# Optimization experiments

Measured on AMD Instinct MI355X. Metric: run time of the kernel, lower is better.

The kernel has to match this reference:

```python
import jax, jax.numpy as jnp
import numpy as np

B, SD, AD, M, MAXC = 65536, 32, 1, 32, 2  # batch, state_dim, action_dim, msg_dim, max_children


def _l2norm(x):
    # F.normalize(x, dim=-1) with eps=1e-12
    return x / jnp.maximum(jnp.linalg.norm(x, axis=-1, keepdims=True), 1e-12)


def _mlp(x, w1, b1, w2, b2, w3, b3):
    # MLPBase: Linear->ReLU->Linear->ReLU->Linear (400/300 hidden)
    h = jax.nn.relu(x @ w1 + b1)
    h = jax.nn.relu(h @ w2 + b2)
    return h @ w3 + b3


def setup_inputs() -> dict:
    key = jax.random.key(0)
    ks = iter(jax.random.split(key, 40))

    def p(shape):
        return jax.random.normal(next(ks), shape, jnp.float32) * 0.05

    inp = {
        "state": jax.random.normal(next(ks), (B, SD), jnp.float32),
        "action": jax.random.normal(next(ks), (B, AD), jnp.float32),
        # CriticUp params
        "up_fc1_w": p((SD + AD, 64)), "up_fc1_b": p((64,)),
        "up_fc2_w": p((64 + M, 64)), "up_fc2_b": p((64,)),
        "up_fc3_w": p((64, M)), "up_fc3_b": p((M,)),
        "att_w": p((9 + SD, M)), "att_b": p((M,)),
    }
    q_in = 12 + M + AD + M   # rel_pos(12) + self_input(msg_dim) + action + msg_down
    m_in = 12 + M + M        # rel_pos(12) + self_input + msg_down
    for n, d, out in (("q1", q_in, 1), ("q2", q_in, 1), ("msg", m_in, M * MAXC)):
        inp[n + "_w1"] = p((d, 400)); inp[n + "_b1"] = p((400,))
        inp[n + "_w2"] = p((400, 300)); inp[n + "_b2"] = p((300,))
        inp[n + "_w3"] = p((300, out)); inp[n + "_b3"] = p((out,))
    return inp


def reference(state, action,
              up_fc1_w, up_fc1_b, up_fc2_w, up_fc2_b, up_fc3_w, up_fc3_b,
              att_w, att_b,
              q1_w1, q1_b1, q1_w2, q1_b2, q1_w3, q1_b3,
              q2_w1, q2_b1, q2_w2, q2_b2, q2_w3, q2_b3,
              msg_w1, msg_b1, msg_w2, msg_b2, msg_w3, msg_b3):
    b = state.shape[0]
    # ---- bottom-up (num_limbs=1: root has no children -> zero child states/messages) ----
    xu = _l2norm(jnp.concatenate([state, action], -1) @ up_fc1_w + up_fc1_b)  # [b,64]
    ch_states = jnp.zeros((b, MAXC, 9 + SD), state.dtype)
    att = jax.nn.softmax(ch_states @ att_w + att_b, axis=-2)                  # [b,MAXC,M]
    m_up = (jnp.zeros((b, MAXC, M), state.dtype) * att).sum(-2)              # [b,M] (zeros)
    h = jnp.tanh(jnp.concatenate([xu, m_up], -1))
    h = jnp.tanh(h @ up_fc2_w + up_fc2_b)
    msg_up = _l2norm(h @ up_fc3_w + up_fc3_b)                                 # [b,M]
    # ---- top-down (root's parent index -1 wraps to itself -> zero relative offsets) ----
    pos = state[:, :3]
    rel = jnp.concatenate([jnp.zeros((b, 6), state.dtype), pos, pos], -1)     # [b,12]
    m_td = jnp.zeros((b, M), state.dtype)                                     # sliced from zero parent_msg
    xum = jnp.concatenate([rel, msg_up, action, m_td], -1)
    x1 = _mlp(xum, q1_w1, q1_b1, q1_w2, q1_b2, q1_w3, q1_b3)                  # [b,1]
    x2 = _mlp(xum, q2_w1, q2_b1, q2_w2, q2_b2, q2_w3, q2_b3)                  # [b,1]
    xm = jnp.tanh(jnp.concatenate([rel, msg_up, m_td], -1))
    msg_down = _l2norm(_mlp(xm, msg_w1, msg_b1, msg_w2, msg_b2, msg_w3, msg_b3))
    del msg_down  # computed per torch forward but unused in single-limb output
    # stack over 1 limb then sum over limb dim == identity
    return (x1, x2)
```

## Files before the change

### kernel.cpp

```cpp
#include <hip/hip_runtime.h>
#include <math.h>


#define BTOT   65536
#define XUM_OFF 655360ull

#define PK_BLK  78
#define PH_THR  512
#define PH_ROWS 128
#define PH_BLK  (BTOT / PH_ROWS)
#define F1W 0
#define F1B 2112
#define F2W 2176
#define F2B 6272
#define F3W 6336
#define F3B 8384
#define W0_FLOATS 8416

#define ML_THR  1024
#define ML_ROWS 128
#define ML_BLK  (BTOT / ML_ROWS)
#define H1S     424

typedef float  f32x4 __attribute__((ext_vector_type(4)));
typedef __bf16 bf16x8 __attribute__((ext_vector_type(8)));
typedef unsigned short u16x8 __attribute__((ext_vector_type(8)));
typedef unsigned short u16x4 __attribute__((ext_vector_type(4)));
typedef unsigned int   u32x2 __attribute__((ext_vector_type(2)));

__device__ __forceinline__ unsigned short f2b(float f) {
  union { float f; unsigned int u; } v; v.f = f;
  return (unsigned short)((v.u + 0x7fffu + ((v.u >> 16) & 1u)) >> 16);
}
__device__ __forceinline__ float b2f(unsigned short u) {
  union { unsigned int u; float f; } v; v.u = ((unsigned int)u) << 16;
  return v.f;
}
__device__ __forceinline__ f32x4 MFMA(bf16x8 a, bf16x8 b, f32x4 c) {
  return __builtin_amdgcn_mfma_f32_16x16x32_bf16(a, b, c, 0, 0, 0);
}
__device__ __forceinline__ bf16x8 ld8(const unsigned short* p) {
  return __builtin_bit_cast(bf16x8, *(const u16x8*)p);
}
__device__ __forceinline__ float ftanh(float x) {
  float e = __builtin_amdgcn_exp2f(x * 2.885390081777927f);
  return (e - 1.0f) * __builtin_amdgcn_rcpf(e + 1.0f);
}

struct P0 {
  const float* state; const float* action;
  const float* f1w; const float* f1b;
  const float* f2w; const float* f2b;
  const float* f3w; const float* f3b;
  const float* q1w1; const float* q1b1; const float* q1w2;
  const float* q2w1; const float* q2b1; const float* q2w2;
  unsigned short* ws;
  unsigned short* xum;
};

__global__ __launch_bounds__(PH_THR, 4) void phase0_kernel(P0 P) {
  __shared__ float w0[W0_FLOATS];
  __shared__ unsigned short hx[PH_ROWS * 68];
  const int tid = threadIdx.x;

  if (blockIdx.x < PK_BLK) {
    const int gid = blockIdx.x * PH_THR + tid;
    const int lane = gid & 63, f = gid >> 6;
    const int q = f / 312, fl = f - q * 312;
    const float* w1 = q ? P.q2w1 : P.q1w1;
    const float* b1 = q ? P.q2b1 : P.q1b1;
    const float* w2 = q ? P.q2w2 : P.q1w2;
    int nt, ks; const bool isw1 = (fl < 52);
    if (isw1) { nt = fl >> 1; ks = fl & 1; }
    else      { int fl2 = fl - 52; nt = fl2 / 13; ks = fl2 - nt * 13; }
    const int col = nt * 16 + (lane & 15);
    const int k0  = ks * 32 + (lane >> 4) * 8;
    unsigned short v[8];
    #pragma unroll
    for (int j = 0; j < 8; ++j) {
      const int k = k0 + j;
      float x = 0.f;
      if (isw1) {
        if (col < 400) {
          if (k < 39) x = w1[(6 + k) * 400 + col];
          else if (k == 39) x = b1[col];
        }
      } else {
        if (k < 400 && col < 300) x = w2[k * 300 + col];
      }
      v[j] = f2b(x);
    }
    *(u16x8*)(P.ws + (size_t)f * 512 + lane * 8) = *(const u16x8*)v;
    return;
  }

  const int row = tid >> 2, sub = tid & 3, j0 = sub * 16;
  const long grow = (long)(blockIdx.x - PK_BLK) * PH_ROWS + row;

  for (int i = tid; i < 528;  i += PH_THR) *(f32x4*)(w0 + F1W + 4*i) = *(const f32x4*)(P.f1w + 4*i);
  for (int i = tid; i < 16;   i += PH_THR) *(f32x4*)(w0 + F1B + 4*i) = *(const f32x4*)(P.f1b + 4*i);
  for (int i = tid; i < 1024; i += PH_THR) *(f32x4*)(w0 + F2W + 4*i) = *(const f32x4*)(P.f2w + 4*i);
  for (int i = tid; i < 16;   i += PH_THR) *(f32x4*)(w0 + F2B + 4*i) = *(const f32x4*)(P.f2b + 4*i);
  for (int i = tid; i < 512;  i += PH_THR) *(f32x4*)(w0 + F3W + 4*i) = *(const f32x4*)(P.f3w + 4*i);
  for (int i = tid; i < 8;    i += PH_THR) *(f32x4*)(w0 + F3B + 4*i) = *(const f32x4*)(P.f3b + 4*i);

  float sa[33];
  {
    const float4* sp = (const float4*)(P.state + grow * 32);
    #pragma unroll
    for (int c = 0; c < 8; ++c) {
      float4 v = sp[c];
      sa[c*4+0] = v.x; sa[c*4+1] = v.y; sa[c*4+2] = v.z; sa[c*4+3] = v.w;
    }
    sa[32] = P.action[grow];
  }
  __syncthreads();

  float acc[16];
  #pragma unroll
  for (int j = 0; j < 16; ++j) acc[j] = w0[F1B + j0 + j];
  #pragma unroll 4
  for (int i = 0; i < 33; ++i) {
    const float s = sa[i];
    const f32x4* wr = (const f32x4*)&w0[F1W + i * 64 + j0];
    #pragma unroll
    for (int c = 0; c < 4; ++c) {
      f32x4 wv = wr[c];
      acc[c*4+0] += s * wv[0]; acc[c*4+1] += s * wv[1];
      acc[c*4+2] += s * wv[2]; acc[c*4+3] += s * wv[3];
    }
  }
  {
    float ss = 0.f;
    #pragma unroll
    for (int j = 0; j < 16; ++j) ss += acc[j] * acc[j];
    ss += __shfl_xor(ss, 1, 64); ss += __shfl_xor(ss, 2, 64);
    const float sc = 1.f / fmaxf(sqrtf(ss), 1e-12f);
    #pragma unroll
    for (int j = 0; j < 16; ++j) hx[row * 68 + j0 + j] = f2b(ftanh(acc[j] * sc));
  }
  __syncthreads();
  #pragma unroll
  for (int j = 0; j < 16; ++j) acc[j] = w0[F2B + j0 + j];
  #pragma unroll 4
  for (int i0 = 0; i0 < 16; ++i0) {
    const u16x4 hv4 = *(const u16x4*)&hx[row * 68 + i0 * 4];
    #pragma unroll
    for (int u = 0; u < 4; ++u) {
      const float hv = b2f(hv4[u]);
      const f32x4* wr = (const f32x4*)&w0[F2W + (i0 * 4 + u) * 64 + j0];
      #pragma unroll
      for (int c = 0; c < 4; ++c) {
        f32x4 wv = wr[c];
        acc[c*4+0] += hv * wv[0]; acc[c*4+1] += hv * wv[1];
        acc[c*4+2] += hv * wv[2]; acc[c*4+3] += hv * wv[3];
      }
    }
  }
  __syncthreads();
  #pragma unroll
  for (int j = 0; j < 16; ++j) hx[row * 68 + j0 + j] = f2b(ftanh(acc[j]));
  __syncthreads();
  const int j0m = sub * 8;
  float am[8];
  #pragma unroll
  for (int j = 0; j < 8; ++j) am[j] = w0[F3B + j0m + j];
  #pragma unroll 4
  for (int i0 = 0; i0 < 16; ++i0) {
    const u16x4 hv4 = *(const u16x4*)&hx[row * 68 + i0 * 4];
    #pragma unroll
    for (int u = 0; u < 4; ++u) {
      const float hv = b2f(hv4[u]);
      const f32x4* wr = (const f32x4*)&w0[F3W + (i0 * 4 + u) * 32 + j0m];
      #pragma unroll
      for (int c = 0; c < 2; ++c) {
        f32x4 wv = wr[c];
        am[c*4+0] += hv * wv[0]; am[c*4+1] += hv * wv[1];
        am[c*4+2] += hv * wv[2]; am[c*4+3] += hv * wv[3];
      }
    }
  }
  float sm = 0.f;
  #pragma unroll
  for (int j = 0; j < 8; ++j) sm += am[j] * am[j];
  sm += __shfl_xor(sm, 1, 64); sm += __shfl_xor(sm, 2, 64);
  const float scm = 1.f / fmaxf(sqrtf(sm), 1e-12f);
  __syncthreads();
  #pragma unroll
  for (int j = 0; j < 8; ++j) hx[row * 68 + j0m + j] = f2b(am[j] * scm);
  __syncthreads();
  {
    u16x8 v0, v1;
    #pragma unroll
    for (int t = 0; t < 16; ++t) {
      const int c = j0 + t;
      unsigned short u;
      if      (c < 3)  u = f2b(sa[c]);
      else if (c < 6)  u = f2b(sa[c - 3]);
      else if (c < 38) u = hx[row * 68 + (c - 6)];
      else if (c == 38) u = f2b(sa[32]);
      else if (c == 39) u = 0x3f80;
      else              u = 0;
      if (t < 8) v0[t] = u; else v1[t - 8] = u;
    }
    unsigned short* dst = P.xum + (size_t)grow * 64 + j0;
    *(u16x8*)dst = v0;
    *(u16x8*)(dst + 8) = v1;
  }
}

struct P1 {
  const unsigned short* img; const unsigned short* xum;
  const float* q1b2; const float* q1w3; const float* q1b3;
  const float* q2b2; const float* q2w3; const float* q2b3;
  float* out;
};

__global__ __launch_bounds__(ML_THR) void mlp_kernel(P1 P) {
  __shared__ __align__(16) unsigned short h1[ML_ROWS * H1S];
  __shared__ float xred[ML_ROWS * 4];

  const int tid  = threadIdx.x;
  const int lane = tid & 63, w = tid >> 6;
  const int rl = lane & 15, g = lane >> 4;

  const int r1 = w & 7, ch = w >> 3;
  const int wm = w >> 2, wn = w & 3;

  const unsigned short* xr = P.xum + ((size_t)blockIdx.x * ML_ROWS + r1 * 16 + rl) * 64;
  const bf16x8 af0 = ld8(xr + g * 8);
  const bf16x8 af1 = ld8(xr + 32 + g * 8);

  for (int q = 0; q < 2; ++q) {
    {
      const unsigned short* w1f = P.img + ((size_t)(q * 312 + ch * 26)) * 512 + lane * 8;
      unsigned short* h1w = &h1[(size_t)(r1 * 16 + rl) * H1S + ch * 208 + g * 4];
      #pragma unroll 4
      for (int t = 0; t < 13; ++t) {
        const bf16x8 b0 = ld8(w1f + (size_t)(t * 2) * 512);
        const bf16x8 b1 = ld8(w1f + (size_t)(t * 2 + 1) * 512);
        f32x4 a = (f32x4){0.f, 0.f, 0.f, 0.f};
        a = MFMA(b0, af0, a);
        a = MFMA(b1, af1, a);
        const float c0 = fmaxf(a[0], 0.f), c1 = fmaxf(a[1], 0.f);
        const float c2 = fmaxf(a[2], 0.f), c3 = fmaxf(a[3], 0.f);
        unsigned int p01, p23;
        asm("v_cvt_pk_bf16_f32 %0, %1, %2" : "=v"(p01) : "v"(c0), "v"(c1));
        asm("v_cvt_pk_bf16_f32 %0, %1, %2" : "=v"(p23) : "v"(c2), "v"(c3));
        u32x2 pk; pk[0] = p01; pk[1] = p23;
        *(u32x2*)(h1w + t * 16) = pk;
      }
    }
    __syncthreads();

    f32x4 acc2[2][5];
    #pragma unroll
    for (int mt = 0; mt < 2; ++mt)
      #pragma unroll
      for (int jn = 0; jn < 5; ++jn) acc2[mt][jn] = (f32x4){0.f, 0.f, 0.f, 0.f};
    {
      const unsigned short* w2f = P.img + ((size_t)(q * 312 + 52 + wn * 65)) * 512 + lane * 8;
      #pragma unroll 2
      for (int ks = 0; ks < 13; ++ks) {
        const bf16x8 a0 = ld8(&h1[(size_t)(wm * 32 + rl) * H1S + ks * 32 + g * 8]);
        const bf16x8 a1 = ld8(&h1[(size_t)(wm * 32 + 16 + rl) * H1S + ks * 32 + g * 8]);
        #pragma unroll
        for (int jn = 0; jn < 5; ++jn) {
          const bf16x8 b = ld8(w2f + (size_t)(jn * 13 + ks) * 512);
          acc2[0][jn] = MFMA(a0, b, acc2[0][jn]);
          acc2[1][jn] = MFMA(a1, b, acc2[1][jn]);
        }
      }
    }

    const float* b2p = q ? P.q2b2 : P.q1b2;
    const float* w3  = q ? P.q2w3 : P.q1w3;
    const float* b3  = q ? P.q2b3 : P.q1b3;
    float xp[2][4];
    #pragma unroll
    for (int mt = 0; mt < 2; ++mt)
      #pragma unroll
      for (int i = 0; i < 4; ++i) xp[mt][i] = 0.f;
    #pragma unroll
    for (int jn = 0; jn < 5; ++jn) {
      const int n = wn * 80 + jn * 16 + rl;
      if (n < 300) {
        const float bv = b2p[n], wv = w3[n];
        #pragma unroll
        for (int mt = 0; mt < 2; ++mt)
          #pragma unroll
          for (int i = 0; i < 4; ++i)
            xp[mt][i] += fmaxf(acc2[mt][jn][i] + bv, 0.f) * wv;
      }
    }
    #pragma unroll
    for (int off = 1; off < 16; off <<= 1)
      #pragma unroll
      for (int mt = 0; mt < 2; ++mt)
        #pragma unroll
        for (int i = 0; i < 4; ++i)
          xp[mt][i] += __shfl_xor(xp[mt][i], off, 64);
    if (rl == 0) {
      #pragma unroll
      for (int mt = 0; mt < 2; ++mt)
        #pragma unroll
        for (int i = 0; i < 4; ++i)
          xred[(wm * 32 + mt * 16 + g * 4 + i) * 4 + wn] = xp[mt][i];
    }
    __syncthreads();
    if (tid < ML_ROWS) {
      const float4 xv = *(const float4*)&xred[tid * 4];
      P.out[(size_t)q * BTOT + (size_t)blockIdx.x * ML_ROWS + tid] =
          xv.x + xv.y + xv.z + xv.w + b3[0];
    }
    __syncthreads();
  }
}

extern "C" void kernel_launch(void* const* d_in, const int* in_sizes, int n_in,
                              void* d_out, int out_size, void* d_ws, size_t ws_size,
                              hipStream_t stream) {
  (void)in_sizes; (void)n_in; (void)out_size; (void)ws_size;
  P0 A;
  A.state  = (const float*)d_in[0];
  A.action = (const float*)d_in[1];
  A.f1w = (const float*)d_in[2]; A.f1b = (const float*)d_in[3];
  A.f2w = (const float*)d_in[4]; A.f2b = (const float*)d_in[5];
  A.f3w = (const float*)d_in[6]; A.f3b = (const float*)d_in[7];
  A.q1w1 = (const float*)d_in[10]; A.q1b1 = (const float*)d_in[11]; A.q1w2 = (const float*)d_in[12];
  A.q2w1 = (const float*)d_in[16]; A.q2b1 = (const float*)d_in[17]; A.q2w2 = (const float*)d_in[18];
  A.ws  = (unsigned short*)d_ws;
  A.xum = (unsigned short*)((unsigned char*)d_ws + XUM_OFF);
  phase0_kernel<<<dim3(PK_BLK + PH_BLK), dim3(PH_THR), 0, stream>>>(A);

  P1 B;
  B.img  = (const unsigned short*)d_ws;
  B.xum  = (const unsigned short*)((unsigned char*)d_ws + XUM_OFF);
  B.q1b2 = (const float*)d_in[13]; B.q1w3 = (const float*)d_in[14]; B.q1b3 = (const float*)d_in[15];
  B.q2b2 = (const float*)d_in[19]; B.q2w3 = (const float*)d_in[20]; B.q2b3 = (const float*)d_in[21];
  B.out  = (float*)d_out;
  mlp_kernel<<<dim3(ML_BLK), dim3(ML_THR), 0, stream>>>(B);
}
```

Before: 112.2 us.

## Fuse bottom-up stage with Q-head MLPs and split hidden layer in K halves

```diff
diff --git a/kernel.cpp b/kernel.cpp
--- a/kernel.cpp
+++ b/kernel.cpp
@@ -3,24 +3,22 @@
 
 
 #define BTOT   65536
-#define XUM_OFF 655360ull
-
-#define PK_BLK  78
-#define PH_THR  512
-#define PH_ROWS 128
-#define PH_BLK  (BTOT / PH_ROWS)
+#define NTHR   512
+#define TBROWS 128
+#define NBLK   (BTOT / TBROWS)
+
+#define O_HX   33664
+#define O_XRED 58368
+#define O_XUM  60416
+#define SMEM_SZ 77824
+#define H1S    228
+
 #define F1W 0
 #define F1B 2112
 #define F2W 2176
 #define F2B 6272
 #define F3W 6336
 #define F3B 8384
-#define W0_FLOATS 8416
-
-#define ML_THR  1024
-#define ML_ROWS 128
-#define ML_BLK  (BTOT / ML_ROWS)
-#define H1S     424
 
 typedef float  f32x4 __attribute__((ext_vector_type(4)));
 typedef __bf16 bf16x8 __attribute__((ext_vector_type(8)));
@@ -47,62 +45,73 @@
   return (e - 1.0f) * __builtin_amdgcn_rcpf(e + 1.0f);
 }
 
-struct P0 {
+struct PackP {
+  const float* q1w1; const float* q1b1; const float* q1w2;
+  const float* q2w1; const float* q2b1; const float* q2w2;
+  unsigned short* ws;
+};
+
+__global__ void pack_weights(PackP P) {
+  const int gid = blockIdx.x * 512 + threadIdx.x;
+  const int lane = gid & 63, f = gid >> 6;
+  const int q = f / 312, fl = f - q * 312;
+  const float* w1 = q ? P.q2w1 : P.q1w1;
+  const float* b1 = q ? P.q2b1 : P.q1b1;
+  const float* w2 = q ? P.q2w2 : P.q1w2;
+  int nt, ks; const bool isw1 = (fl < 52);
+  if (isw1) { nt = fl >> 1; ks = fl & 1; }
+  else      { int fl2 = fl - 52; nt = fl2 / 13; ks = fl2 - nt * 13; }
+  const int col = nt * 16 + (lane & 15);
+  const int k0  = ks * 32 + (lane >> 4) * 8;
+  unsigned short v[8];
+  #pragma unroll
+  for (int j = 0; j < 8; ++j) {
+    const int k = k0 + j;
+    float x = 0.f;
+    if (isw1) {
+      if (col < 400) {
+        if (k < 39) x = w1[(6 + k) * 400 + col];
+        else if (k == 39) x = b1[col];
+      }
+    } else {
+      if (k < 400 && col < 300) x = w2[k * 300 + col];
+    }
+    v[j] = f2b(x);
+  }
+  *(u16x8*)(P.ws + (size_t)f * 512 + lane * 8) = *(const u16x8*)v;
+}
+
+struct FP {
   const float* state; const float* action;
   const float* f1w; const float* f1b;
   const float* f2w; const float* f2b;
   const float* f3w; const float* f3b;
-  const float* q1w1; const float* q1b1; const float* q1w2;
-  const float* q2w1; const float* q2b1; const float* q2w2;
-  unsigned short* ws;
-  unsigned short* xum;
+  const unsigned short* img;
+  const float* q1b2; const float* q1w3; const float* q1b3;
+  const float* q2b2; const float* q2w3; const float* q2b3;
+  float* out;
 };
 
-__global__ __launch_bounds__(PH_THR, 4) void phase0_kernel(P0 P) {
-  __shared__ float w0[W0_FLOATS];
-  __shared__ unsigned short hx[PH_ROWS * 68];
-  const int tid = threadIdx.x;
-
-  if (blockIdx.x < PK_BLK) {
-    const int gid = blockIdx.x * PH_THR + tid;
-    const int lane = gid & 63, f = gid >> 6;
-    const int q = f / 312, fl = f - q * 312;
-    const float* w1 = q ? P.q2w1 : P.q1w1;
-    const float* b1 = q ? P.q2b1 : P.q1b1;
-    const float* w2 = q ? P.q2w2 : P.q1w2;
-    int nt, ks; const bool isw1 = (fl < 52);
-    if (isw1) { nt = fl >> 1; ks = fl & 1; }
-    else      { int fl2 = fl - 52; nt = fl2 / 13; ks = fl2 - nt * 13; }
-    const int col = nt * 16 + (lane & 15);
-    const int k0  = ks * 32 + (lane >> 4) * 8;
-    unsigned short v[8];
-    #pragma unroll
-    for (int j = 0; j < 8; ++j) {
-      const int k = k0 + j;
-      float x = 0.f;
-      if (isw1) {
-        if (col < 400) {
-          if (k < 39) x = w1[(6 + k) * 400 + col];
-          else if (k == 39) x = b1[col];
-        }
-      } else {
-        if (k < 400 && col < 300) x = w2[k * 300 + col];
-      }
-      v[j] = f2b(x);
-    }
-    *(u16x8*)(P.ws + (size_t)f * 512 + lane * 8) = *(const u16x8*)v;
-    return;
-  }
-
+__global__ __launch_bounds__(NTHR, 2) void critic_fused(FP P) {
+  __shared__ __align__(16) unsigned char smem[SMEM_SZ];
+  float*          w0   = (float*)smem;
+  unsigned short* hx   = (unsigned short*)(smem + O_HX);
+  unsigned short* h1   = (unsigned short*)smem;
+  float*          xred = (float*)(smem + O_XRED);
+  unsigned short* xumL = (unsigned short*)(smem + O_XUM);
+
+  const int tid  = threadIdx.x;
+  const int lane = tid & 63, w = tid >> 6;
+  const int rl = lane & 15, g = lane >> 4;
   const int row = tid >> 2, sub = tid & 3, j0 = sub * 16;
-  const long grow = (long)(blockIdx.x - PK_BLK) * PH_ROWS + row;
-
-  for (int i = tid; i < 528;  i += PH_THR) *(f32x4*)(w0 + F1W + 4*i) = *(const f32x4*)(P.f1w + 4*i);
-  for (int i = tid; i < 16;   i += PH_THR) *(f32x4*)(w0 + F1B + 4*i) = *(const f32x4*)(P.f1b + 4*i);
-  for (int i = tid; i < 1024; i += PH_THR) *(f32x4*)(w0 + F2W + 4*i) = *(const f32x4*)(P.f2w + 4*i);
-  for (int i = tid; i < 16;   i += PH_THR) *(f32x4*)(w0 + F2B + 4*i) = *(const f32x4*)(P.f2b + 4*i);
-  for (int i = tid; i < 512;  i += PH_THR) *(f32x4*)(w0 + F3W + 4*i) = *(const f32x4*)(P.f3w + 4*i);
-  for (int i = tid; i < 8;    i += PH_THR) *(f32x4*)(w0 + F3B + 4*i) = *(const f32x4*)(P.f3b + 4*i);
+  const long grow = (long)blockIdx.x * TBROWS + row;
+
+  for (int i = tid; i < 528;  i += NTHR) *(f32x4*)(w0 + F1W + 4*i) = *(const f32x4*)(P.f1w + 4*i);
+  for (int i = tid; i < 16;   i += NTHR) *(f32x4*)(w0 + F1B + 4*i) = *(const f32x4*)(P.f1b + 4*i);
+  for (int i = tid; i < 1024; i += NTHR) *(f32x4*)(w0 + F2W + 4*i) = *(const f32x4*)(P.f2w + 4*i);
+  for (int i = tid; i < 16;   i += NTHR) *(f32x4*)(w0 + F2B + 4*i) = *(const f32x4*)(P.f2b + 4*i);
+  for (int i = tid; i < 512;  i += NTHR) *(f32x4*)(w0 + F3W + 4*i) = *(const f32x4*)(P.f3w + 4*i);
+  for (int i = tid; i < 8;    i += NTHR) *(f32x4*)(w0 + F3B + 4*i) = *(const f32x4*)(P.f3b + 4*i);
 
   float sa[33];
   {
@@ -162,9 +171,9 @@
   for (int j = 0; j < 16; ++j) hx[row * 68 + j0 + j] = f2b(ftanh(acc[j]));
   __syncthreads();
   const int j0m = sub * 8;
-  float am[8];
-  #pragma unroll
-  for (int j = 0; j < 8; ++j) am[j] = w0[F3B + j0m + j];
+  float am8[8];
+  #pragma unroll
+  for (int j = 0; j < 8; ++j) am8[j] = w0[F3B + j0m + j];
   #pragma unroll 4
   for (int i0 = 0; i0 < 16; ++i0) {
     const u16x4 hv4 = *(const u16x4*)&hx[row * 68 + i0 * 4];
@@ -175,19 +184,19 @@
       #pragma unroll
       for (int c = 0; c < 2; ++c) {
         f32x4 wv = wr[c];
-        am[c*4+0] += hv * wv[0]; am[c*4+1] += hv * wv[1];
-        am[c*4+2] += hv * wv[2]; am[c*4+3] += hv * wv[3];
+        am8[c*4+0] += hv * wv[0]; am8[c*4+1] += hv * wv[1];
+        am8[c*4+2] += hv * wv[2]; am8[c*4+3] += hv * wv[3];
       }
     }
   }
   float sm = 0.f;
   #pragma unroll
-  for (int j = 0; j < 8; ++j) sm += am[j] * am[j];
+  for (int j = 0; j < 8; ++j) sm += am8[j] * am8[j];
   sm += __shfl_xor(sm, 1, 64); sm += __shfl_xor(sm, 2, 64);
   const float scm = 1.f / fmaxf(sqrtf(sm), 1e-12f);
   __syncthreads();
   #pragma unroll
-  for (int j = 0; j < 8; ++j) hx[row * 68 + j0m + j] = f2b(am[j] * scm);
+  for (int j = 0; j < 8; ++j) hx[row * 68 + j0m + j] = f2b(am8[j] * scm);
   __syncthreads();
   {
     u16x8 v0, v1;
@@ -203,82 +212,80 @@
       else              u = 0;
       if (t < 8) v0[t] = u; else v1[t - 8] = u;
     }
-    unsigned short* dst = P.xum + (size_t)grow * 64 + j0;
+    unsigned short* dst = &xumL[row * 68 + j0];
     *(u16x8*)dst = v0;
     *(u16x8*)(dst + 8) = v1;
   }
-}
-
-struct P1 {
-  const unsigned short* img; const unsigned short* xum;
-  const float* q1b2; const float* q1w3; const float* q1b3;
-  const float* q2b2; const float* q2w3; const float* q2b3;
-  float* out;
-};
-
-__global__ __launch_bounds__(ML_THR) void mlp_kernel(P1 P) {
-  __shared__ __align__(16) unsigned short h1[ML_ROWS * H1S];
-  __shared__ float xred[ML_ROWS * 4];
-
-  const int tid  = threadIdx.x;
-  const int lane = tid & 63, w = tid >> 6;
-  const int rl = lane & 15, g = lane >> 4;
-
-  const int r1 = w & 7, ch = w >> 3;
-  const int wm = w >> 2, wn = w & 3;
-
-  const unsigned short* xr = P.xum + ((size_t)blockIdx.x * ML_ROWS + r1 * 16 + rl) * 64;
+  __syncthreads();
+
+  const unsigned short* xr = &xumL[(w * 16 + rl) * 68];
   const bf16x8 af0 = ld8(xr + g * 8);
   const bf16x8 af1 = ld8(xr + 32 + g * 8);
+  __syncthreads();
+
+  const int wm = w >> 2, wn = w & 3;
 
   for (int q = 0; q < 2; ++q) {
-    {
-      const unsigned short* w1f = P.img + ((size_t)(q * 312 + ch * 26)) * 512 + lane * 8;
-      unsigned short* h1w = &h1[(size_t)(r1 * 16 + rl) * H1S + ch * 208 + g * 4];
-      #pragma unroll 4
-      for (int t = 0; t < 13; ++t) {
-        const bf16x8 b0 = ld8(w1f + (size_t)(t * 2) * 512);
-        const bf16x8 b1 = ld8(w1f + (size_t)(t * 2 + 1) * 512);
-        f32x4 a = (f32x4){0.f, 0.f, 0.f, 0.f};
-        a = MFMA(b0, af0, a);
-        a = MFMA(b1, af1, a);
-        const float c0 = fmaxf(a[0], 0.f), c1 = fmaxf(a[1], 0.f);
-        const float c2 = fmaxf(a[2], 0.f), c3 = fmaxf(a[3], 0.f);
-        unsigned int p01, p23;
-        asm("v_cvt_pk_bf16_f32 %0, %1, %2" : "=v"(p01) : "v"(c0), "v"(c1));
-        asm("v_cvt_pk_bf16_f32 %0, %1, %2" : "=v"(p23) : "v"(c2), "v"(c3));
-        u32x2 pk; pk[0] = p01; pk[1] = p23;
-        *(u32x2*)(h1w + t * 16) = pk;
-      }
-    }
-    __syncthreads();
-
-    f32x4 acc2[2][5];
-    #pragma unroll
-    for (int mt = 0; mt < 2; ++mt)
+    f32x4 acc2[4][5];
+    #pragma unroll
+    for (int mt = 0; mt < 4; ++mt)
       #pragma unroll
       for (int jn = 0; jn < 5; ++jn) acc2[mt][jn] = (f32x4){0.f, 0.f, 0.f, 0.f};
-    {
-      const unsigned short* w2f = P.img + ((size_t)(q * 312 + 52 + wn * 65)) * 512 + lane * 8;
-      #pragma unroll 2
-      for (int ks = 0; ks < 13; ++ks) {
-        const bf16x8 a0 = ld8(&h1[(size_t)(wm * 32 + rl) * H1S + ks * 32 + g * 8]);
-        const bf16x8 a1 = ld8(&h1[(size_t)(wm * 32 + 16 + rl) * H1S + ks * 32 + g * 8]);
-        #pragma unroll
-        for (int jn = 0; jn < 5; ++jn) {
-          const bf16x8 b = ld8(w2f + (size_t)(jn * 13 + ks) * 512);
-          acc2[0][jn] = MFMA(a0, b, acc2[0][jn]);
-          acc2[1][jn] = MFMA(a1, b, acc2[1][jn]);
+
+    #pragma unroll
+    for (int kh = 0; kh < 2; ++kh) {
+      const int NTk = kh ? 12 : 14;
+      const int KSk = kh ? 6 : 7;
+      const int NTO = kh ? 14 : 0;
+      const int KSO = kh ? 7 : 0;
+
+      {
+        const unsigned short* w1f = P.img + ((size_t)(q * 312 + NTO * 2)) * 512 + lane * 8;
+        unsigned short* h1w = &h1[(size_t)(w * 16 + rl) * H1S + g * 4];
+        #pragma unroll 2
+        for (int t = 0; t < NTk; ++t) {
+          const bf16x8 b0 = ld8(w1f + (size_t)(t * 2) * 512);
+          const bf16x8 b1 = ld8(w1f + (size_t)(t * 2 + 1) * 512);
+          f32x4 a = (f32x4){0.f, 0.f, 0.f, 0.f};
+          a = MFMA(b0, af0, a);
+          a = MFMA(b1, af1, a);
+          const float c0 = fmaxf(a[0], 0.f), c1 = fmaxf(a[1], 0.f);
+          const float c2 = fmaxf(a[2], 0.f), c3 = fmaxf(a[3], 0.f);
+          unsigned int p01, p23;
+          asm("v_cvt_pk_bf16_f32 %0, %1, %2" : "=v"(p01) : "v"(c0), "v"(c1));
+          asm("v_cvt_pk_bf16_f32 %0, %1, %2" : "=v"(p23) : "v"(c2), "v"(c3));
+          u32x2 pk; pk[0] = p01; pk[1] = p23;
+          *(u32x2*)(h1w + t * 16) = pk;
         }
       }
+      __syncthreads();
+
+      {
+        const unsigned short* w2f = P.img + ((size_t)(q * 312 + 52 + wn * 65)) * 512 + lane * 8;
+        for (int ks = 0; ks < KSk; ++ks) {
+          const int ksg = KSO + ks;
+          bf16x8 am[4];
+          #pragma unroll
+          for (int mt = 0; mt < 4; ++mt)
+            am[mt] = ld8(&h1[(size_t)(wm * 64 + mt * 16 + rl) * H1S + ks * 32 + g * 8]);
+          #pragma unroll
+          for (int jn = 0; jn < 5; ++jn) {
+            const bf16x8 b = ld8(w2f + (size_t)(jn * 13 + ksg) * 512);
+            #pragma unroll
+            for (int mt = 0; mt < 4; ++mt)
+              acc2[mt][jn] = MFMA(am[mt], b, acc2[mt][jn]);
+          }
+        }
+      }
+      __syncthreads();
     }
 
     const float* b2p = q ? P.q2b2 : P.q1b2;
     const float* w3  = q ? P.q2w3 : P.q1w3;
     const float* b3  = q ? P.q2b3 : P.q1b3;
-    float xp[2][4];
-    #pragma unroll
-    for (int mt = 0; mt < 2; ++mt)
+    float xp[4][4];
+    #pragma unroll
+    for (int mt = 0; mt < 4; ++mt)
       #pragma unroll
       for (int i = 0; i < 4; ++i) xp[mt][i] = 0.f;
     #pragma unroll
@@ -287,7 +294,7 @@
       if (n < 300) {
         const float bv = b2p[n], wv = w3[n];
         #pragma unroll
-        for (int mt = 0; mt < 2; ++mt)
+        for (int mt = 0; mt < 4; ++mt)
           #pragma unroll
           for (int i = 0; i < 4; ++i)
             xp[mt][i] += fmaxf(acc2[mt][jn][i] + bv, 0.f) * wv;
@@ -296,21 +303,21 @@
     #pragma unroll
     for (int off = 1; off < 16; off <<= 1)
       #pragma unroll
-      for (int mt = 0; mt < 2; ++mt)
+      for (int mt = 0; mt < 4; ++mt)
         #pragma unroll
         for (int i = 0; i < 4; ++i)
           xp[mt][i] += __shfl_xor(xp[mt][i], off, 64);
     if (rl == 0) {
       #pragma unroll
-      for (int mt = 0; mt < 2; ++mt)
+      for (int mt = 0; mt < 4; ++mt)
         #pragma unroll
         for (int i = 0; i < 4; ++i)
-          xred[(wm * 32 + mt * 16 + g * 4 + i) * 4 + wn] = xp[mt][i];
+          xred[(wm * 64 + mt * 16 + g * 4 + i) * 4 + wn] = xp[mt][i];
     }
     __syncthreads();
-    if (tid < ML_ROWS) {
+    if (tid < TBROWS) {
       const float4 xv = *(const float4*)&xred[tid * 4];
-      P.out[(size_t)q * BTOT + (size_t)blockIdx.x * ML_ROWS + tid] =
+      P.out[(size_t)q * BTOT + (size_t)blockIdx.x * TBROWS + tid] =
           xv.x + xv.y + xv.z + xv.w + b3[0];
     }
     __syncthreads();
@@ -321,23 +328,21 @@
                               void* d_out, int out_size, void* d_ws, size_t ws_size,
                               hipStream_t stream) {
   (void)in_sizes; (void)n_in; (void)out_size; (void)ws_size;
-  P0 A;
-  A.state  = (const float*)d_in[0];
-  A.action = (const float*)d_in[1];
-  A.f1w = (const float*)d_in[2]; A.f1b = (const float*)d_in[3];
-  A.f2w = (const float*)d_in[4]; A.f2b = (const float*)d_in[5];
-  A.f3w = (const float*)d_in[6]; A.f3b = (const float*)d_in[7];
-  A.q1w1 = (const float*)d_in[10]; A.q1b1 = (const float*)d_in[11]; A.q1w2 = (const float*)d_in[12];
-  A.q2w1 = (const float*)d_in[16]; A.q2b1 = (const float*)d_in[17]; A.q2w2 = (const float*)d_in[18];
-  A.ws  = (unsigned short*)d_ws;
-  A.xum = (unsigned short*)((unsigned char*)d_ws + XUM_OFF);
-  phase0_kernel<<<dim3(PK_BLK + PH_BLK), dim3(PH_THR), 0, stream>>>(A);
-
-  P1 B;
-  B.img  = (const unsigned short*)d_ws;
-  B.xum  = (const unsigned short*)((unsigned char*)d_ws + XUM_OFF);
-  B.q1b2 = (const float*)d_in[13]; B.q1w3 = (const float*)d_in[14]; B.q1b3 = (const float*)d_in[15];
-  B.q2b2 = (const float*)d_in[19]; B.q2w3 = (const float*)d_in[20]; B.q2b3 = (const float*)d_in[21];
-  B.out  = (float*)d_out;
-  mlp_kernel<<<dim3(ML_BLK), dim3(ML_THR), 0, stream>>>(B);
-}
+  PackP K;
+  K.q1w1 = (const float*)d_in[10]; K.q1b1 = (const float*)d_in[11]; K.q1w2 = (const float*)d_in[12];
+  K.q2w1 = (const float*)d_in[16]; K.q2b1 = (const float*)d_in[17]; K.q2w2 = (const float*)d_in[18];
+  K.ws   = (unsigned short*)d_ws;
+  pack_weights<<<dim3(78), dim3(512), 0, stream>>>(K);
+
+  FP P;
+  P.state  = (const float*)d_in[0];
+  P.action = (const float*)d_in[1];
+  P.f1w = (const float*)d_in[2]; P.f1b = (const float*)d_in[3];
+  P.f2w = (const float*)d_in[4]; P.f2b = (const float*)d_in[5];
+  P.f3w = (const float*)d_in[6]; P.f3b = (const float*)d_in[7];
+  P.img  = (const unsigned short*)d_ws;
+  P.q1b2 = (const float*)d_in[13]; P.q1w3 = (const float*)d_in[14]; P.q1b3 = (const float*)d_in[15];
+  P.q2b2 = (const float*)d_in[19]; P.q2w3 = (const float*)d_in[20]; P.q2b3 = (const float*)d_in[21];
+  P.out  = (float*)d_out;
+  critic_fused<<<dim3(NBLK), dim3(NTHR), 0, stream>>>(P);
+}
```

Measured after the change: 129.2 us. +15.2%, slower.
